# Kernel tuning notes

Measured on AMD Instinct MI355X. Metric: run time of the kernel, lower is better.

## Reference

```python
import jax, jax.numpy as jnp
import numpy as np

HIDDEN = 2304
N_HEADS = 8
N_KV_HEADS = 4
HEAD_DIM = 256
SLIDING_WINDOW = 4096
QUERY_PRE_ATTN_SCALAR = 256.0
SOFTCAP = 50.0
ROPE_BASE = 10000.0


def setup_inputs() -> dict:
    key = jax.random.key(0)
    ks = jax.random.split(key, 6)
    B, S = 1, 4096
    scale = 0.02
    return {
        "hidden_states": jax.random.normal(ks[0], (B, S, HIDDEN), dtype=jnp.float32),
        "Wq": jax.random.normal(ks[1], (HIDDEN, N_HEADS * HEAD_DIM), dtype=jnp.float32) * scale,
        "Wk": jax.random.normal(ks[2], (HIDDEN, N_KV_HEADS * HEAD_DIM), dtype=jnp.float32) * scale,
        "Wv": jax.random.normal(ks[3], (HIDDEN, N_KV_HEADS * HEAD_DIM), dtype=jnp.float32) * scale,
        "Wo": jax.random.normal(ks[4], (N_HEADS * HEAD_DIM, HIDDEN), dtype=jnp.float32) * scale,
        "position_ids": jnp.arange(S, dtype=jnp.int64 if jax.config.jax_enable_x64 else jnp.int32)[None, :],
    }


def _rope_cos_sin(position_ids):
    # inv_freq: (head_dim//2,)
    inv_freq = 1.0 / (ROPE_BASE ** (jnp.arange(0, HEAD_DIM, 2, dtype=jnp.float32) / HEAD_DIM))
    freqs = position_ids.astype(jnp.float32)[..., None] * inv_freq[None, None, :]  # (B,S,hd/2)
    emb = jnp.concatenate([freqs, freqs], axis=-1)  # (B,S,hd)
    return jnp.cos(emb), jnp.sin(emb)


def _rotate_half(x):
    x1, x2 = jnp.split(x, 2, axis=-1)
    return jnp.concatenate([-x2, x1], axis=-1)


def reference(hidden_states, Wq, Wk, Wv, Wo, position_ids):
    B, S, _ = hidden_states.shape
    cos, sin = _rope_cos_sin(position_ids)  # (B,S,hd)
    cos = cos[:, None]  # (B,1,S,hd) broadcast over heads
    sin = sin[:, None]

    q = (hidden_states @ Wq).reshape(B, S, N_HEADS, HEAD_DIM).transpose(0, 2, 1, 3)
    k = (hidden_states @ Wk).reshape(B, S, N_KV_HEADS, HEAD_DIM).transpose(0, 2, 1, 3)
    v = (hidden_states @ Wv).reshape(B, S, N_KV_HEADS, HEAD_DIM).transpose(0, 2, 1, 3)

    q = q * cos + _rotate_half(q) * sin
    k = k * cos + _rotate_half(k) * sin

    # GQA: repeat kv heads to match query heads
    n_rep = N_HEADS // N_KV_HEADS
    k = jnp.repeat(k, n_rep, axis=1)  # (B,H,S,hd)
    v = jnp.repeat(v, n_rep, axis=1)

    scaling = QUERY_PRE_ATTN_SCALAR ** -0.5
    scores = jnp.einsum("bhqd,bhkd->bhqk", q, k) * scaling

    # attention logit softcapping
    scores = SOFTCAP * jnp.tanh(scores / SOFTCAP)

    # causal + sliding window mask
    qi = jnp.arange(S)[:, None]
    kj = jnp.arange(S)[None, :]
    mask = (kj <= qi) & (qi - kj < SLIDING_WINDOW)  # (S,S)
    scores = jnp.where(mask[None, None], scores, jnp.asarray(-1e30, scores.dtype))

    attn = jax.nn.softmax(scores, axis=-1)
    ctx = jnp.einsum("bhqk,bhkd->bhqd", attn, v)  # (B,H,S,hd)
    ctx = ctx.transpose(0, 2, 1, 3).reshape(B, S, N_HEADS * HEAD_DIM)
    return ctx @ Wo
```

## Files before the change

kernel.cpp:

```cpp
#include <hip/hip_runtime.h>
#include <cstdint>
#include <cstddef>

typedef unsigned short u16;
typedef short bf16x8 __attribute__((ext_vector_type(8)));
typedef float f32x4 __attribute__((ext_vector_type(4)));

#define S_LEN 4096
#define HID   2304
#define NH    8
#define NKV   4
#define HD    256
#define QD    2048
#define KD    1024
#define QKVW  4096
#define CHT   32
#define SLOTS_PER_HEAD 160

__device__ __forceinline__ u16 f2b(float f) {
    union { float f; uint32_t u; } v; v.f = f;
    uint32_t r = (v.u + 0x7FFFu + ((v.u >> 16) & 1u)) >> 16;
    return (u16)r;
}
__device__ __forceinline__ float b2f(u16 u) {
    union { uint32_t u; float f; } v; v.u = ((uint32_t)u) << 16;
    return v.f;
}

__device__ __forceinline__ void glds16(const void* g, void* l) {
    __builtin_amdgcn_global_load_lds(
        (__attribute__((address_space(1))) void*)(const_cast<void*>(g)),
        (__attribute__((address_space(3))) void*)l, 16, 0, 0);
}

__device__ __forceinline__ int slot_base(int qt) {
    int a = qt >> 4, b = qt & 15;
    return (a + 1) * (8 * a + b);
}

__device__ __forceinline__ float softcap_p(float s) {
    float u = s * 0.00125f;
    u = fminf(fmaxf(u, -0.53f), 0.53f);
    float u2 = u * u;
    float t50 = u * (50.0f + u2 * (-16.6666667f + 6.66666667f * u2));
    return __expf(t50);
}

__global__ __launch_bounds__(256) void cvt_h(const float* __restrict__ in, u16* __restrict__ out, int n4) {
    int id = blockIdx.x * 256 + threadIdx.x;
    if (id >= n4) return;
    float4 v = ((const float4*)in)[id];
    uint2 o;
    o.x = (uint32_t)f2b(v.x) | ((uint32_t)f2b(v.y) << 16);
    o.y = (uint32_t)f2b(v.z) | ((uint32_t)f2b(v.w) << 16);
    ((uint2*)out)[id] = o;
}

__device__ __forceinline__ void twcvt_body(const float* __restrict__ W, u16* __restrict__ out,
                                           int K, int N, int ldo, int n0, int k0) {
    __shared__ float T[64][68];
    const int t = threadIdx.x;
    for (int i = 0; i < 4; i++) {
        int id = i * 256 + t;
        int r = id >> 4, c4 = id & 15;
        float4 v = *(const float4*)(W + (size_t)(k0 + r) * N + n0 + c4 * 4);
        *(float4*)(&T[r][c4 * 4]) = v;
    }
    __syncthreads();
    for (int i = 0; i < 4; i++) {
        int id = i * 256 + t;
        int rn = id >> 4, c4 = id & 15;
        u16 a = f2b(T[c4 * 4 + 0][rn]);
        u16 b = f2b(T[c4 * 4 + 1][rn]);
        u16 c = f2b(T[c4 * 4 + 2][rn]);
        u16 d = f2b(T[c4 * 4 + 3][rn]);
        uint2 o;
        o.x = (uint32_t)a | ((uint32_t)b << 16);
        o.y = (uint32_t)c | ((uint32_t)d << 16);
        *(uint2*)(out + (size_t)(n0 + rn) * ldo + k0 + c4 * 4) = o;
    }
}

__global__ __launch_bounds__(256) void twcvt(const float* __restrict__ W, u16* __restrict__ out,
                                             int K, int N, int ldo) {
    twcvt_body(W, out, K, N, ldo, blockIdx.x * 64, blockIdx.y * 64);
}

__global__ __launch_bounds__(256) void twcvt_qkv(const float* __restrict__ Wq,
                                                 const float* __restrict__ Wk,
                                                 const float* __restrict__ Wv,
                                                 u16* __restrict__ out) {
    const int z = blockIdx.z;
    const float* W = (z == 0) ? Wq : (z == 1) ? Wk : Wv;
    const int N = (z == 0) ? QD : KD;
    const int n0 = blockIdx.x * 64;
    if (n0 >= N) return;
    u16* ob = out + ((z == 0) ? 0 : (z == 1) ? (size_t)QD * HID : (size_t)(QD + KD) * HID);
    twcvt_body(W, ob, HID, N, HID, n0, blockIdx.y * 64);
}

template<int BF16_OUT>
__global__ __launch_bounds__(512, 2) void gemm256(const u16* __restrict__ A, const u16* __restrict__ B,
                                                  void* __restrict__ Cp, int M, int N, int K) {
    const int tid = threadIdx.x;
    const int wv = tid >> 6, lane = tid & 63;
    const int quad = lane >> 4, m16 = lane & 15;
    const int gx = gridDim.x;
    int bid = blockIdx.y * gx + blockIdx.x;
    const int cpx = (gx * gridDim.y) >> 3;
    bid = (bid & 7) * cpx + (bid >> 3);
    const int m0 = (bid / gx) * 256, n0 = (bid % gx) * 256;
    const int wm = (wv & 1) * 128, wn = (wv >> 1) * 64;

    __shared__ __align__(16) u16 As[2][256 * 64];
    __shared__ __align__(16) u16 Bs[2][256 * 64];

    const int lr = lane >> 3, ls = lane & 7;
    const int scol = ((ls ^ lr) << 3);
    const u16* pA[4]; const u16* pB[4];
    int du[4];
#pragma unroll
    for (int j = 0; j < 4; j++) {
        int u = wv + 8 * j;
        pA[j] = A + (size_t)(m0 + u * 8 + lr) * K + scol;
        pB[j] = B + (size_t)(n0 + u * 8 + lr) * K + scol;
        du[j] = u * 512;
    }

    f32x4 acc[8][4];
#pragma unroll
    for (int i = 0; i < 8; i++)
#pragma unroll
        for (int j = 0; j < 4; j++) acc[i][j] = (f32x4){0.f, 0.f, 0.f, 0.f};

    const int aBase = (wm + m16) * 64;
    const int bBase = (wn + m16) * 64;
    const int s0 = ((quad ^ (m16 & 7)) << 3);
    const int s1 = s0 ^ 32;

    const int NT = K >> 6;
#pragma unroll
    for (int j = 0; j < 4; j++) glds16(pA[j], &As[0][du[j]]);
#pragma unroll
    for (int j = 0; j < 4; j++) glds16(pB[j], &Bs[0][du[j]]);
    asm volatile("s_waitcnt vmcnt(0)" ::: "memory");
    __builtin_amdgcn_sched_barrier(0);
    __builtin_amdgcn_s_barrier();

    for (int t = 0; t < NT; t++) {
        const int cur = t & 1, nxt = cur ^ 1;
        const int kn = (t + 1) << 6;
        const bool pre = (t + 1 < NT);
        bf16x8 af[4], bf[4];

#define MFMA16(IOFF)                                                               \
        _Pragma("unroll")                                                          \
        for (int i = 0; i < 4; i++)                                                \
            _Pragma("unroll")                                                      \
            for (int j = 0; j < 4; j++)                                            \
                acc[i + (IOFF)][j] =                                               \
                    __builtin_amdgcn_mfma_f32_16x16x32_bf16(af[i], bf[j],          \
                                                            acc[i + (IOFF)][j], 0, 0, 0);
#define PHASE_SYNC()                                                               \
        __builtin_amdgcn_s_barrier();                                              \
        asm volatile("s_waitcnt lgkmcnt(0)" ::: "memory");                         \
        __builtin_amdgcn_sched_barrier(0);

#pragma unroll
        for (int i = 0; i < 4; i++) af[i] = *(const bf16x8*)(&As[cur][aBase + i * 1024 + s0]);
#pragma unroll
        for (int j = 0; j < 4; j++) bf[j] = *(const bf16x8*)(&Bs[cur][bBase + j * 1024 + s0]);
        if (pre) {
#pragma unroll
            for (int j = 0; j < 4; j++) glds16(pA[j] + kn, &As[nxt][du[j]]);
        }
        PHASE_SYNC();
        __builtin_amdgcn_s_setprio(1);
        MFMA16(0);
        __builtin_amdgcn_s_setprio(0);
        __builtin_amdgcn_s_barrier();
#pragma unroll
        for (int i = 0; i < 4; i++) af[i] = *(const bf16x8*)(&As[cur][aBase + (i + 4) * 1024 + s0]);
        if (pre) {
#pragma unroll
            for (int j = 0; j < 4; j++) glds16(pB[j] + kn, &Bs[nxt][du[j]]);
        }
        PHASE_SYNC();
        __builtin_amdgcn_s_setprio(1);
        MFMA16(4);
        __builtin_amdgcn_s_setprio(0);
        __builtin_amdgcn_s_barrier();
#pragma unroll
        for (int i = 0; i < 4; i++) af[i] = *(const bf16x8*)(&As[cur][aBase + i * 1024 + s1]);
#pragma unroll
        for (int j = 0; j < 4; j++) bf[j] = *(const bf16x8*)(&Bs[cur][bBase + j * 1024 + s1]);
        PHASE_SYNC();
        __builtin_amdgcn_s_setprio(1);
        MFMA16(0);
        __builtin_amdgcn_s_setprio(0);
        __builtin_amdgcn_s_barrier();
#pragma unroll
        for (int i = 0; i < 4; i++) af[i] = *(const bf16x8*)(&As[cur][aBase + (i + 4) * 1024 + s1]);
        PHASE_SYNC();
        __builtin_amdgcn_s_setprio(1);
        MFMA16(4);
        __builtin_amdgcn_s_setprio(0);
        asm volatile("s_waitcnt vmcnt(0)" ::: "memory");
        __builtin_amdgcn_sched_barrier(0);
        __builtin_amdgcn_s_barrier();
#undef MFMA16
#undef PHASE_SYNC
    }
#pragma unroll
    for (int i = 0; i < 8; i++)
#pragma unroll
        for (int j = 0; j < 4; j++)
#pragma unroll
            for (int r = 0; r < 4; r++) {
                int row = m0 + wm + i * 16 + quad * 4 + r;
                int col = n0 + wn + j * 16 + m16;
                if (BF16_OUT) ((u16*)Cp)[(size_t)row * N + col] = f2b(acc[i][j][r]);
                else          ((float*)Cp)[(size_t)row * N + col] = acc[i][j][r];
            }
}

template<int BF16_OUT>
__global__ __launch_bounds__(256, 2) void gemm_bt(const u16* __restrict__ A, const u16* __restrict__ B,
                                                  void* __restrict__ Cp, int M, int N, int K) {
    const int tid  = threadIdx.x;
    const int wv = tid >> 6, lane = tid & 63;
    const int quad = lane >> 4, m16 = lane & 15;
    const int gx = gridDim.x;
    int bid = blockIdx.y * gx + blockIdx.x;
    const int cpx = (gx * gridDim.y) >> 3;
    bid = (bid & 7) * cpx + (bid >> 3);
    const int m0 = (bid / gx) * 128, n0 = (bid % gx) * 128;
    const int wm = (wv & 1) * 64, wn = (wv >> 1) * 64;
    __shared__ __align__(16) u16 As[128 * 32];
    __shared__ __align__(16) u16 Bs[128 * 32];
    int s0i = (wv * 2) * 64 + lane, s1i = s0i + 64;
    int row0 = s0i >> 2, c0 = (s0i & 3) ^ (row0 & 3);
    int row1 = s1i >> 2, c1 = (s1i & 3) ^ (row1 & 3);
    const u16* pA0 = A + (size_t)(m0 + row0) * K + c0 * 8;
    const u16* pA1 = A + (size_t)(m0 + row1) * K + c1 * 8;
    const u16* pB0 = B + (size_t)(n0 + row0) * K + c0 * 8;
    const u16* pB1 = B + (size_t)(n0 + row1) * K + c1 * 8;
    u16* lA0 = &As[(wv * 2 + 0) * 512]; u16* lA1 = &As[(wv * 2 + 1) * 512];
    u16* lB0 = &Bs[(wv * 2 + 0) * 512]; u16* lB1 = &Bs[(wv * 2 + 1) * 512];

    const f32x4 z4 = {0.f, 0.f, 0.f, 0.f};
    f32x4 acc00 = z4, acc01 = z4, acc02 = z4, acc03 = z4;
    f32x4 acc10 = z4, acc11 = z4, acc12 = z4, acc13 = z4;
    f32x4 acc20 = z4, acc21 = z4, acc22 = z4, acc23 = z4;
    f32x4 acc30 = z4, acc31 = z4, acc32 = z4, acc33 = z4;

    const int sw = quad ^ (m16 & 3);
    const u16* ra0 = &As[(wm + 0 * 16 + m16) * 32 + (sw << 3)];
    const u16* ra1 = &As[(wm + 1 * 16 + m16) * 32 + (sw << 3)];
    const u16* ra2 = &As[(wm + 2 * 16 + m16) * 32 + (sw << 3)];
    const u16* ra3 = &As[(wm + 3 * 16 + m16) * 32 + (sw << 3)];
    const u16* rb0 = &Bs[(wn + 0 * 16 + m16) * 32 + (sw << 3)];
    const u16* rb1 = &Bs[(wn + 1 * 16 + m16) * 32 + (sw << 3)];
    const u16* rb2 = &Bs[(wn + 2 * 16 + m16) * 32 + (sw << 3)];
    const u16* rb3 = &Bs[(wn + 3 * 16 + m16) * 32 + (sw << 3)];

    for (int k0 = 0; k0 < K; k0 += 32) {
        __syncthreads();
        glds16(pA0 + k0, lA0);
        glds16(pA1 + k0, lA1);
        glds16(pB0 + k0, lB0);
        glds16(pB1 + k0, lB1);
        __syncthreads();
        bf16x8 af0 = *(const bf16x8*)ra0, af1 = *(const bf16x8*)ra1;
        bf16x8 af2 = *(const bf16x8*)ra2, af3 = *(const bf16x8*)ra3;
        bf16x8 bf0 = *(const bf16x8*)rb0, bf1 = *(const bf16x8*)rb1;
        bf16x8 bf2 = *(const bf16x8*)rb2, bf3 = *(const bf16x8*)rb3;
        acc00 = __builtin_amdgcn_mfma_f32_16x16x32_bf16(af0, bf0, acc00, 0, 0, 0);
        acc01 = __builtin_amdgcn_mfma_f32_16x16x32_bf16(af0, bf1, acc01, 0, 0, 0);
        acc02 = __builtin_amdgcn_mfma_f32_16x16x32_bf16(af0, bf2, acc02, 0, 0, 0);
        acc03 = __builtin_amdgcn_mfma_f32_16x16x32_bf16(af0, bf3, acc03, 0, 0, 0);
        acc10 = __builtin_amdgcn_mfma_f32_16x16x32_bf16(af1, bf0, acc10, 0, 0, 0);
        acc11 = __builtin_amdgcn_mfma_f32_16x16x32_bf16(af1, bf1, acc11, 0, 0, 0);
        acc12 = __builtin_amdgcn_mfma_f32_16x16x32_bf16(af1, bf2, acc12, 0, 0, 0);
        acc13 = __builtin_amdgcn_mfma_f32_16x16x32_bf16(af1, bf3, acc13, 0, 0, 0);
        acc20 = __builtin_amdgcn_mfma_f32_16x16x32_bf16(af2, bf0, acc20, 0, 0, 0);
        acc21 = __builtin_amdgcn_mfma_f32_16x16x32_bf16(af2, bf1, acc21, 0, 0, 0);
        acc22 = __builtin_amdgcn_mfma_f32_16x16x32_bf16(af2, bf2, acc22, 0, 0, 0);
        acc23 = __builtin_amdgcn_mfma_f32_16x16x32_bf16(af2, bf3, acc23, 0, 0, 0);
        acc30 = __builtin_amdgcn_mfma_f32_16x16x32_bf16(af3, bf0, acc30, 0, 0, 0);
        acc31 = __builtin_amdgcn_mfma_f32_16x16x32_bf16(af3, bf1, acc31, 0, 0, 0);
        acc32 = __builtin_amdgcn_mfma_f32_16x16x32_bf16(af3, bf2, acc32, 0, 0, 0);
        acc33 = __builtin_amdgcn_mfma_f32_16x16x32_bf16(af3, bf3, acc33, 0, 0, 0);
    }

#define STORE_TILE(I, J, ACC)                                              \
    {                                                                      \
        _Pragma("unroll")                                                  \
        for (int r = 0; r < 4; r++) {                                      \
            int row = m0 + wm + (I) * 16 + quad * 4 + r;                   \
            int col = n0 + wn + (J) * 16 + m16;                            \
            float v = (ACC)[r];                                            \
            if (BF16_OUT) ((u16*)Cp)[(size_t)row * N + col] = f2b(v);      \
            else          ((float*)Cp)[(size_t)row * N + col] = v;         \
        }                                                                  \
    }
    STORE_TILE(0, 0, acc00) STORE_TILE(0, 1, acc01) STORE_TILE(0, 2, acc02) STORE_TILE(0, 3, acc03)
    STORE_TILE(1, 0, acc10) STORE_TILE(1, 1, acc11) STORE_TILE(1, 2, acc12) STORE_TILE(1, 3, acc13)
    STORE_TILE(2, 0, acc20) STORE_TILE(2, 1, acc21) STORE_TILE(2, 2, acc22) STORE_TILE(2, 3, acc23)
    STORE_TILE(3, 0, acc30) STORE_TILE(3, 1, acc31) STORE_TILE(3, 2, acc32) STORE_TILE(3, 3, acc33)
#undef STORE_TILE
}

__global__ __launch_bounds__(256) void rope_k(const u16* __restrict__ QKV, const int* __restrict__ pos,
                                              u16* __restrict__ Qb, u16* __restrict__ Kb) {
    int id = blockIdx.x * 256 + threadIdx.x;
    const int NQ = S_LEN * NH * 128;
    const u16* src; u16* dst;
    int s, j;
    if (id < NQ) {
        s = id >> 10; int rem = id & 1023; int h = rem >> 7; j = rem & 127;
        src = QKV + (size_t)s * QKVW + h * 256;
        dst = Qb + (size_t)s * QD + h * 256;
    } else {
        int id2 = id - NQ;
        s = id2 >> 9; int rem = id2 & 511; int kvh = rem >> 7; j = rem & 127;
        src = QKV + (size_t)s * QKVW + QD + kvh * 256;
        dst = Kb + (size_t)s * KD + kvh * 256;
    }
    float p = (float)pos[s];
    float invf = expf(-0.07195578429985445f * (float)j);
    float ang = p * invf;
    float sn, cs;
    sincosf(ang, &sn, &cs);
    float x1 = b2f(src[j]), x2 = b2f(src[j + 128]);
    dst[j]       = f2b(x1 * cs - x2 * sn);
    dst[j + 128] = f2b(x2 * cs + x1 * sn);
}

__global__ __launch_bounds__(256) void vtrans(const u16* __restrict__ QKV, u16* __restrict__ Vt) {
    const int s0 = blockIdx.x * 64, d0 = blockIdx.y * 64;
    __shared__ u16 T[64][72];
    const int t = threadIdx.x;
    for (int i = 0; i < 2; i++) {
        int id = i * 256 + t;
        int r = id >> 3, c = id & 7;
        uint4 v = *(const uint4*)(QKV + (size_t)(s0 + r) * QKVW + (QD + KD) + d0 + c * 8);
        *(uint4*)(&T[r][c * 8]) = v;
    }
    __syncthreads();
    for (int i = 0; i < 2; i++) {
        int id = i * 256 + t;
        int r = id >> 3, c = id & 7;
        union { u16 u[8]; uint4 v; } o;
        for (int jj = 0; jj < 8; jj++) o.u[jj] = T[c * 8 + jj][r];
        *(uint4*)(Vt + (size_t)(d0 + r) * S_LEN + s0 + c * 8) = o.v;
    }
}

__global__ __launch_bounds__(256, 3) void attn_part(const u16* __restrict__ Qb, const u16* __restrict__ Kb,
                                                    const u16* __restrict__ Vt,
                                                    u16* __restrict__ Part, float* __restrict__ Lpart) {
    const int tid  = threadIdx.x;
    const int wv = tid >> 6, lane = tid & 63;
    const int quad = lane >> 4, m16 = lane & 15;
    const int qt = blockIdx.x, h = blockIdx.y, ch = blockIdx.z;
    const int n_kvt = 2 * qt + 2;
    const int t0 = ch * CHT;
    if (t0 >= n_kvt) return;
    const int t1 = min(t0 + CHT, n_kvt);
    const int kvh = h >> 1;
    const int q0 = qt * 64;
    const int slot = h * SLOTS_PER_HEAD + slot_base(qt) + ch;

    __shared__ __align__(16) u16 Kl[2][32 * 256];
    __shared__ __align__(16) u16 Vl[256 * 32];
    __shared__ __align__(16) u16 Pl[4][16 * 32];

    int kOff[4], vOff[4];
#pragma unroll
    for (int i = 0; i < 4; i++) {
        int s = (wv * 4 + i) * 64 + lane;
        int kv = s >> 5, c = (s & 31) ^ (kv & 7);
        kOff[i] = kv * KD + c * 8;
        int d = s >> 2, cc = (s & 3) ^ ((d >> 1) & 3);
        vOff[i] = d * S_LEN + cc * 8;
    }
    const u16* Kbase = Kb + kvh * 256;
    const u16* Vbase = Vt + (size_t)(kvh * 256) * S_LEN;

    bf16x8 qf[8];
    {
        const u16* qp = Qb + (size_t)(q0 + wv * 16 + m16) * QD + h * 256 + quad * 8;
#pragma unroll
        for (int ks = 0; ks < 8; ks++) qf[ks] = *(const bf16x8*)(qp + ks * 32);
    }
    float li[4] = {0.f, 0.f, 0.f, 0.f};
    f32x4 o[4][4];
#pragma unroll
    for (int i = 0; i < 4; i++)
#pragma unroll
        for (int j = 0; j < 4; j++) o[i][j] = (f32x4){0.f, 0.f, 0.f, 0.f};

#pragma unroll
    for (int i = 0; i < 4; i++)
        glds16(Kbase + kOff[i] + t0 * (32 * KD), &Kl[0][(wv * 4 + i) * 512]);

    for (int kt = t0; kt < t1; kt++) {
        const int cur = (kt - t0) & 1, nxt = cur ^ 1;
        asm volatile("s_waitcnt vmcnt(0)" ::: "memory");
        __builtin_amdgcn_sched_barrier(0);
        __builtin_amdgcn_s_barrier();
#pragma unroll
        for (int i = 0; i < 4; i++)
            glds16(Vbase + vOff[i] + kt * 32, &Vl[(wv * 4 + i) * 512]);
        if (kt + 1 < t1) {
#pragma unroll
            for (int i = 0; i < 4; i++)
                glds16(Kbase + kOff[i] + (kt + 1) * (32 * KD), &Kl[nxt][(wv * 4 + i) * 512]);
        }
        f32x4 s[2];
#pragma unroll
        for (int nt = 0; nt < 2; nt++) {
            f32x4 a = (f32x4){0.f, 0.f, 0.f, 0.f};
            int kr = nt * 16 + m16;
            int sw = kr & 7;
#pragma unroll
            for (int ks = 0; ks < 8; ks++) {
                int c = ks * 4 + quad;
                bf16x8 kf = *(const bf16x8*)(&Kl[cur][kr * 256 + ((c ^ sw) << 3)]);
                a = __builtin_amdgcn_mfma_f32_16x16x32_bf16(qf[ks], kf, a, 0, 0, 0);
            }
            s[nt] = a;
        }
        const int kvb = kt * 32;
        u16* Pw = &Pl[wv][0];
#pragma unroll
        for (int nt = 0; nt < 2; nt++)
#pragma unroll
            for (int r = 0; r < 4; r++) {
                float p = softcap_p(s[nt][r]);
                int kvg = kvb + nt * 16 + m16;
                int qg  = q0 + wv * 16 + quad * 4 + r;
                p = (kvg > qg) ? 0.f : p;
                li[r] += p;
                int m = quad * 4 + r;
                int c = 2 * nt + (m16 >> 3);
                int off = m16 & 7;
                Pw[m * 32 + ((c ^ ((m >> 1) & 3)) << 3) + off] = f2b(p);
            }
        if (kt + 1 < t1) {
            asm volatile("s_waitcnt vmcnt(4) lgkmcnt(0)" ::: "memory");
        } else {
            asm volatile("s_waitcnt vmcnt(0) lgkmcnt(0)" ::: "memory");
        }
        __builtin_amdgcn_sched_barrier(0);
        __builtin_amdgcn_s_barrier();
        bf16x8 pf[4];
#pragma unroll
        for (int qs = 0; qs < 4; qs++)
            pf[qs] = *(const bf16x8*)(&Pl[qs][m16 * 32 + ((quad ^ ((m16 >> 1) & 3)) << 3)]);
#pragma unroll
        for (int dt = 0; dt < 4; dt++) {
            int d = wv * 64 + dt * 16 + m16;
            bf16x8 vf = *(const bf16x8*)(&Vl[d * 32 + ((quad ^ ((d >> 1) & 3)) << 3)]);
            o[0][dt] = __builtin_amdgcn_mfma_f32_16x16x32_bf16(pf[0], vf, o[0][dt], 0, 0, 0);
            o[1][dt] = __builtin_amdgcn_mfma_f32_16x16x32_bf16(pf[1], vf, o[1][dt], 0, 0, 0);
            o[2][dt] = __builtin_amdgcn_mfma_f32_16x16x32_bf16(pf[2], vf, o[2][dt], 0, 0, 0);
            o[3][dt] = __builtin_amdgcn_mfma_f32_16x16x32_bf16(pf[3], vf, o[3][dt], 0, 0, 0);
        }
    }
    u16* Pp = Part + (size_t)slot * (64 * 256);
#pragma unroll
    for (int qs = 0; qs < 4; qs++)
#pragma unroll
        for (int dt = 0; dt < 4; dt++)
#pragma unroll
            for (int r = 0; r < 4; r++)
                Pp[(qs * 16 + quad * 4 + r) * 256 + wv * 64 + dt * 16 + m16] = f2b(o[qs][dt][r]);
#pragma unroll
    for (int r = 0; r < 4; r++) {
        float l = li[r];
        l += __shfl_xor(l, 1); l += __shfl_xor(l, 2);
        l += __shfl_xor(l, 4); l += __shfl_xor(l, 8);
        if (m16 == 0) Lpart[slot * 64 + wv * 16 + quad * 4 + r] = l;
    }
}

__global__ __launch_bounds__(256) void attn_combine(const u16* __restrict__ Part,
                                                    const float* __restrict__ Lpart,
                                                    u16* __restrict__ Ctx) {
    const int qt = blockIdx.x, h = blockIdx.y;
    const int nch = (qt >> 4) + 1;
    const int slot0 = h * SLOTS_PER_HEAD + slot_base(qt);
    const int t = threadIdx.x;
    const int q0 = qt * 64;
    __shared__ float linv[64];
    if (t < 64) {
        float l = 0.f;
        for (int c = 0; c < nch; c++) l += Lpart[(slot0 + c) * 64 + t];
        linv[t] = 1.f / l;
    }
    __syncthreads();
    const u16* P0 = Part + (size_t)slot0 * (64 * 256);
    for (int i = 0; i < 8; i++) {
        int idx = i * 256 + t;
        int row = idx >> 5, c8 = idx & 31;
        float acc[8] = {0.f,0.f,0.f,0.f,0.f,0.f,0.f,0.f};
        for (int c = 0; c < nch; c++) {
            uint4 v = *(const uint4*)(P0 + (size_t)c * (64 * 256) + row * 256 + c8 * 8);
            uint32_t w[4] = {v.x, v.y, v.z, v.w};
            for (int k = 0; k < 4; k++) {
                acc[k * 2]     += b2f((u16)(w[k] & 0xFFFF));
                acc[k * 2 + 1] += b2f((u16)(w[k] >> 16));
            }
        }
        float iv = linv[row];
        uint4 ov;
        uint32_t* op = (uint32_t*)&ov;
        for (int k = 0; k < 4; k++)
            op[k] = (uint32_t)f2b(acc[k * 2] * iv) | ((uint32_t)f2b(acc[k * 2 + 1] * iv) << 16);
        *(uint4*)(Ctx + (size_t)(q0 + row) * QD + h * 256 + c8 * 8) = ov;
    }
}

extern "C" void kernel_launch(void* const* d_in, const int* in_sizes, int n_in,
                              void* d_out, int out_size, void* d_ws, size_t ws_size,
                              hipStream_t stream) {
    const float* H  = (const float*)d_in[0];
    const float* Wq = (const float*)d_in[1];
    const float* Wk = (const float*)d_in[2];
    const float* Wv = (const float*)d_in[3];
    const float* Wo = (const float*)d_in[4];
    const int* pos  = (const int*)d_in[5];
    float* out = (float*)d_out;

    char* ws = (char*)d_ws;
    size_t off = 0;
    u16* Hb     = (u16*)(ws + off); off += (size_t)S_LEN * HID * 2;
    u16* Wqkvt  = (u16*)(ws + off); off += (size_t)QKVW * HID * 2;
    u16* Wot    = (u16*)(ws + off); off += (size_t)HID * QD * 2;
    u16* QKVraw = (u16*)(ws + off); off += (size_t)S_LEN * QKVW * 2;
    u16* Qb     = (u16*)(ws + off); off += (size_t)S_LEN * QD * 2;
    u16* Kb     = (u16*)(ws + off); off += (size_t)S_LEN * KD * 2;
    u16* Vt     = (u16*)(ws + off); off += (size_t)KD * S_LEN * 2;
    u16* Ctx    = (u16*)(ws + off); off += (size_t)S_LEN * QD * 2;
    u16* Part   = (u16*)(ws + off);  off += (size_t)NH * SLOTS_PER_HEAD * 64 * 256 * 2;
    float* Lprt = (float*)(ws + off); off += (size_t)NH * SLOTS_PER_HEAD * 64 * 4;

    cvt_h<<<dim3((S_LEN * HID / 4 + 255) / 256), dim3(256), 0, stream>>>(H, Hb, S_LEN * HID / 4);
    twcvt_qkv<<<dim3(32, HID / 64, 3), dim3(256), 0, stream>>>(Wq, Wk, Wv, Wqkvt);
    twcvt<<<dim3(HID / 64, QD / 64), dim3(256), 0, stream>>>(Wo, Wot, QD, HID, QD);
    gemm256<1><<<dim3(QKVW / 256, S_LEN / 256), dim3(512), 0, stream>>>(Hb, Wqkvt, QKVraw, S_LEN, QKVW, HID);
    rope_k<<<dim3((S_LEN * NH * 128 + S_LEN * NKV * 128) / 256), dim3(256), 0, stream>>>(QKVraw, pos, Qb, Kb);
    vtrans<<<dim3(S_LEN / 64, KD / 64), dim3(256), 0, stream>>>(QKVraw, Vt);
    attn_part<<<dim3(64, NH, 4), dim3(256), 0, stream>>>(Qb, Kb, Vt, Part, Lprt);
    attn_combine<<<dim3(64, NH), dim3(256), 0, stream>>>(Part, Lprt, Ctx);
    gemm_bt<0><<<dim3(HID / 128, S_LEN / 128), dim3(256), 0, stream>>>(Ctx, Wot, out, S_LEN, HID, QD);
}
```

Baseline: 447.0 us.

## Share RoPE sincos across heads, skip mask on full tiles, add MFMA priority

The RoPE kernel now has each thread compute one sin/cos pair and apply it to all 8 Q heads and 4 K heads of a position, instead of recomputing it per head. This cuts the transcendental work and the thread count. The attention kernel takes a mask-free softmax path for KV tiles that lie entirely below the diagonal. It also raises wave priority around the MFMA blocks with s_setprio, so matrix work is issued ahead of other waves' softmax work.

```diff
diff --git a/kernel.cpp b/kernel.cpp
--- a/kernel.cpp
+++ b/kernel.cpp
@@ -314,27 +314,28 @@
 __global__ __launch_bounds__(256) void rope_k(const u16* __restrict__ QKV, const int* __restrict__ pos,
                                               u16* __restrict__ Qb, u16* __restrict__ Kb) {
     int id = blockIdx.x * 256 + threadIdx.x;
-    const int NQ = S_LEN * NH * 128;
-    const u16* src; u16* dst;
-    int s, j;
-    if (id < NQ) {
-        s = id >> 10; int rem = id & 1023; int h = rem >> 7; j = rem & 127;
-        src = QKV + (size_t)s * QKVW + h * 256;
-        dst = Qb + (size_t)s * QD + h * 256;
-    } else {
-        int id2 = id - NQ;
-        s = id2 >> 9; int rem = id2 & 511; int kvh = rem >> 7; j = rem & 127;
-        src = QKV + (size_t)s * QKVW + QD + kvh * 256;
-        dst = Kb + (size_t)s * KD + kvh * 256;
-    }
+    int s = id >> 7, j = id & 127;
     float p = (float)pos[s];
     float invf = expf(-0.07195578429985445f * (float)j);
     float ang = p * invf;
     float sn, cs;
     sincosf(ang, &sn, &cs);
-    float x1 = b2f(src[j]), x2 = b2f(src[j + 128]);
-    dst[j]       = f2b(x1 * cs - x2 * sn);
-    dst[j + 128] = f2b(x2 * cs + x1 * sn);
+    const u16* src = QKV + (size_t)s * QKVW;
+    u16* dq = Qb + (size_t)s * QD;
+#pragma unroll
+    for (int h = 0; h < NH; h++) {
+        float x1 = b2f(src[h * 256 + j]), x2 = b2f(src[h * 256 + 128 + j]);
+        dq[h * 256 + j]       = f2b(x1 * cs - x2 * sn);
+        dq[h * 256 + 128 + j] = f2b(x2 * cs + x1 * sn);
+    }
+    const u16* sk = src + QD;
+    u16* dk = Kb + (size_t)s * KD;
+#pragma unroll
+    for (int h = 0; h < NKV; h++) {
+        float x1 = b2f(sk[h * 256 + j]), x2 = b2f(sk[h * 256 + 128 + j]);
+        dk[h * 256 + j]       = f2b(x1 * cs - x2 * sn);
+        dk[h * 256 + 128 + j] = f2b(x2 * cs + x1 * sn);
+    }
 }
 
 __global__ __launch_bounds__(256) void vtrans(const u16* __restrict__ QKV, u16* __restrict__ Vt) {
@@ -419,6 +420,7 @@
                 glds16(Kbase + kOff[i] + (kt + 1) * (32 * KD), &Kl[nxt][(wv * 4 + i) * 512]);
         }
         f32x4 s[2];
+        __builtin_amdgcn_s_setprio(1);
 #pragma unroll
         for (int nt = 0; nt < 2; nt++) {
             f32x4 a = (f32x4){0.f, 0.f, 0.f, 0.f};
@@ -432,22 +434,37 @@
             }
             s[nt] = a;
         }
+        __builtin_amdgcn_s_setprio(0);
         const int kvb = kt * 32;
         u16* Pw = &Pl[wv][0];
-#pragma unroll
-        for (int nt = 0; nt < 2; nt++)
-#pragma unroll
-            for (int r = 0; r < 4; r++) {
-                float p = softcap_p(s[nt][r]);
-                int kvg = kvb + nt * 16 + m16;
-                int qg  = q0 + wv * 16 + quad * 4 + r;
-                p = (kvg > qg) ? 0.f : p;
-                li[r] += p;
-                int m = quad * 4 + r;
-                int c = 2 * nt + (m16 >> 3);
-                int off = m16 & 7;
-                Pw[m * 32 + ((c ^ ((m >> 1) & 3)) << 3) + off] = f2b(p);
-            }
+        if (kvb + 31 <= q0) {
+#pragma unroll
+            for (int nt = 0; nt < 2; nt++)
+#pragma unroll
+                for (int r = 0; r < 4; r++) {
+                    float p = softcap_p(s[nt][r]);
+                    li[r] += p;
+                    int m = quad * 4 + r;
+                    int c = 2 * nt + (m16 >> 3);
+                    int off = m16 & 7;
+                    Pw[m * 32 + ((c ^ ((m >> 1) & 3)) << 3) + off] = f2b(p);
+                }
+        } else {
+#pragma unroll
+            for (int nt = 0; nt < 2; nt++)
+#pragma unroll
+                for (int r = 0; r < 4; r++) {
+                    float p = softcap_p(s[nt][r]);
+                    int kvg = kvb + nt * 16 + m16;
+                    int qg  = q0 + wv * 16 + quad * 4 + r;
+                    p = (kvg > qg) ? 0.f : p;
+                    li[r] += p;
+                    int m = quad * 4 + r;
+                    int c = 2 * nt + (m16 >> 3);
+                    int off = m16 & 7;
+                    Pw[m * 32 + ((c ^ ((m >> 1) & 3)) << 3) + off] = f2b(p);
+                }
+        }
         if (kt + 1 < t1) {
             asm volatile("s_waitcnt vmcnt(4) lgkmcnt(0)" ::: "memory");
         } else {
@@ -459,6 +476,7 @@
 #pragma unroll
         for (int qs = 0; qs < 4; qs++)
             pf[qs] = *(const bf16x8*)(&Pl[qs][m16 * 32 + ((quad ^ ((m16 >> 1) & 3)) << 3)]);
+        __builtin_amdgcn_s_setprio(1);
 #pragma unroll
         for (int dt = 0; dt < 4; dt++) {
             int d = wv * 64 + dt * 16 + m16;
@@ -468,6 +486,7 @@
             o[2][dt] = __builtin_amdgcn_mfma_f32_16x16x32_bf16(pf[2], vf, o[2][dt], 0, 0, 0);
             o[3][dt] = __builtin_amdgcn_mfma_f32_16x16x32_bf16(pf[3], vf, o[3][dt], 0, 0, 0);
         }
+        __builtin_amdgcn_s_setprio(0);
     }
     u16* Pp = Part + (size_t)slot * (64 * 256);
 #pragma unroll
@@ -551,7 +570,7 @@
     twcvt_qkv<<<dim3(32, HID / 64, 3), dim3(256), 0, stream>>>(Wq, Wk, Wv, Wqkvt);
     twcvt<<<dim3(HID / 64, QD / 64), dim3(256), 0, stream>>>(Wo, Wot, QD, HID, QD);
     gemm256<1><<<dim3(QKVW / 256, S_LEN / 256), dim3(512), 0, stream>>>(Hb, Wqkvt, QKVraw, S_LEN, QKVW, HID);
-    rope_k<<<dim3((S_LEN * NH * 128 + S_LEN * NKV * 128) / 256), dim3(256), 0, stream>>>(QKVraw, pos, Qb, Kb);
+    rope_k<<<dim3(S_LEN * 128 / 256), dim3(256), 0, stream>>>(QKVraw, pos, Qb, Kb);
     vtrans<<<dim3(S_LEN / 64, KD / 64), dim3(256), 0, stream>>>(QKVraw, Vt);
     attn_part<<<dim3(64, NH, 4), dim3(256), 0, stream>>>(Qb, Kb, Vt, Part, Lprt);
     attn_combine<<<dim3(64, NH), dim3(256), 0, stream>>>(Part, Lprt, Ctx);
```

After: 428.4 us. -4.1%, faster.
